# Kernel optimization log

Measured on AMD Instinct MI355X. Metric: run time of the kernel, lower is better.

## Reference

```python
import jax, jax.numpy as jnp
import numpy as np

D_MODEL = 2048
N_HEADS = 16
HEAD_DIM = D_MODEL // N_HEADS
ROPE_THETA = 10000.0
B, S = 2, 2048
MAX_POS = 8192


def _rope(x, position_ids):
    # x: [b, h, s, hd]; position_ids: [b, s] int
    half = HEAD_DIM // 2
    inv_freq = 1.0 / (ROPE_THETA ** (jnp.arange(0, HEAD_DIM, 2, dtype=jnp.float32) / HEAD_DIM))  # [half]
    ang = position_ids[..., None].astype(jnp.float32) * inv_freq  # [b, s, half]
    cos = jnp.concatenate([jnp.cos(ang), jnp.cos(ang)], axis=-1)[:, None]  # [b, 1, s, hd]
    sin = jnp.concatenate([jnp.sin(ang), jnp.sin(ang)], axis=-1)[:, None]
    x1, x2 = x[..., :half], x[..., half:]
    rot = jnp.concatenate([-x2, x1], axis=-1)  # rotate_half
    return x * cos + rot * sin


def setup_inputs() -> dict:
    key = jax.random.key(0)
    ks = jax.random.split(key, 6)
    wscale = 1.0 / np.sqrt(D_MODEL)
    x_sparse = jax.random.normal(ks[0], (B, S, D_MODEL), dtype=jnp.float32)
    Wq = jax.random.normal(ks[1], (D_MODEL, D_MODEL), dtype=jnp.float32) * wscale
    Wk = jax.random.normal(ks[2], (D_MODEL, D_MODEL), dtype=jnp.float32) * wscale
    Wv = jax.random.normal(ks[3], (D_MODEL, D_MODEL), dtype=jnp.float32) * wscale
    Wo = jax.random.normal(ks[4], (D_MODEL, D_MODEL), dtype=jnp.float32) * wscale
    position_ids = jnp.sort(jax.random.randint(ks[5], (B, S), 0, MAX_POS), axis=-1).astype(jnp.int64)
    return {"x_sparse": x_sparse, "Wq": Wq, "Wk": Wk, "Wv": Wv, "Wo": Wo, "position_ids": position_ids}


def reference(x_sparse, Wq, Wk, Wv, Wo, position_ids):
    b, s, d = x_sparse.shape

    def heads(W):
        return (x_sparse @ W).reshape(b, s, N_HEADS, HEAD_DIM).transpose(0, 2, 1, 3)  # [b,h,s,hd]

    q = _rope(heads(Wq), position_ids)
    k = _rope(heads(Wk), position_ids)
    v = heads(Wv)

    scores = jnp.einsum('bhqd,bhkd->bhqk', q, k) / np.float32(np.sqrt(HEAD_DIM))
    # dynamic position-based causal mask: pos_i >= pos_j, broadcast over heads
    mask = position_ids[:, None, :, None] >= position_ids[:, None, None, :]  # [b,1,s,s]
    scores = jnp.where(mask, scores, jnp.float32(-1e30))
    attn = jax.nn.softmax(scores, axis=-1)
    out = jnp.einsum('bhqk,bhkd->bhqd', attn, v)  # [b,h,s,hd]
    out = out.transpose(0, 2, 1, 3).reshape(b, s, d)
    return out @ Wo
```

## Files before the change

kernel.cpp:

```cpp
#include <hip/hip_runtime.h>
#include <stdint.h>


typedef unsigned short u16;
typedef unsigned int u32;
typedef __attribute__((ext_vector_type(8))) short bf16x8;
typedef __attribute__((ext_vector_type(4))) float f32x4;

#define SEQ 2048
#define DM 2048
#define NH 16
#define HD 128
#define SM_SCALE 0.08838834764831845f
#define K2LOG 0.12751743f

__device__ __forceinline__ u16 f2bf(float f) {
  union { float f; uint32_t u; } v; v.f = f;
  uint32_t u = v.u + 0x7fffu + ((v.u >> 16) & 1u);
  return (u16)(u >> 16);
}
__device__ __forceinline__ float bf2f(u16 h) {
  union { uint32_t u; float f; } v; v.u = ((uint32_t)h) << 16; return v.f;
}
__device__ __forceinline__ u32 pack2(float a, float b) {
  return (u32)f2bf(a) | ((u32)f2bf(b) << 16);
}
__device__ __forceinline__ u32 pack2_trunc(float a, float b) {
  union { float f; u32 u; } x, y; x.f = a; y.f = b;
  return (x.u >> 16) | (y.u & 0xFFFF0000u);
}

__device__ __forceinline__ void gl2lds16(const void* g, void* l) {
  __builtin_amdgcn_global_load_lds(
      (const __attribute__((address_space(1))) uint32_t*)g,
      (__attribute__((address_space(3))) uint32_t*)l, 16, 0, 0);
}

__global__ __launch_bounds__(256) void cvt_x(const float* __restrict__ x, u16* __restrict__ xb) {
  int i = blockIdx.x * 256 + threadIdx.x;
  float4 v = ((const float4*)x)[i];
  uint2 r;
  r.x = pack2(v.x, v.y);
  r.y = pack2(v.z, v.w);
  ((uint2*)xb)[i] = r;
}

__global__ __launch_bounds__(256) void wtrans(const float* __restrict__ w0, const float* __restrict__ w1,
                                              const float* __restrict__ w2, const float* __restrict__ w3,
                                              u16* __restrict__ dst) {
  const float* W = blockIdx.z == 0 ? w0 : blockIdx.z == 1 ? w1 : blockIdx.z == 2 ? w2 : w3;
  u16* D = dst + (size_t)blockIdx.z * DM * DM;
  int k0 = blockIdx.x * 32, n0 = blockIdx.y * 32;
  __shared__ u16 t[32][33];
  int tx = threadIdx.x, ty = threadIdx.y;
#pragma unroll
  for (int i = 0; i < 32; i += 8)
    t[ty + i][tx] = f2bf(W[(size_t)(k0 + ty + i) * DM + n0 + tx]);
  __syncthreads();
#pragma unroll
  for (int i = 0; i < 32; i += 8)
    D[(size_t)(n0 + ty + i) * DM + k0 + tx] = t[tx][ty + i];
}

__device__ __forceinline__ void gemm_core(const u16* __restrict__ A, const u16* __restrict__ Bt,
                                          int m0, int n0, u16* As, u16* Bs, f32x4 acc[4][4]) {
  int tid = threadIdx.x, lane = tid & 63;
  int l15 = lane & 15, quad = lane >> 4;
  int wave = tid >> 6;
  int wm = (wave >> 1) * 64, wn = (wave & 1) * 64;
  for (int k0 = 0; k0 < DM; k0 += 64) {
#pragma unroll
    for (int i = 0; i < 4; ++i) {
      int s = i * 256 + tid;
      int row = s >> 3, c = (s & 7) ^ (row & 7);
      gl2lds16(&A[(size_t)(m0 + row) * DM + k0 + c * 8], &As[(s & ~63) * 8]);
      gl2lds16(&Bt[(size_t)(n0 + row) * DM + k0 + c * 8], &Bs[(s & ~63) * 8]);
    }
    __syncthreads();
#pragma unroll
    for (int kk = 0; kk < 2; ++kk) {
      bf16x8 af[4], bfr[4];
#pragma unroll
      for (int mt = 0; mt < 4; ++mt) {
        int row = wm + mt * 16 + l15;
        int c = (kk * 4 + quad) ^ (row & 7);
        af[mt] = *(const bf16x8*)&As[row * 64 + c * 8];
      }
#pragma unroll
      for (int nt = 0; nt < 4; ++nt) {
        int row = wn + nt * 16 + l15;
        int c = (kk * 4 + quad) ^ (row & 7);
        bfr[nt] = *(const bf16x8*)&Bs[row * 64 + c * 8];
      }
#pragma unroll
      for (int mt = 0; mt < 4; ++mt)
#pragma unroll
        for (int nt = 0; nt < 4; ++nt)
          acc[mt][nt] = __builtin_amdgcn_mfma_f32_16x16x32_bf16(af[mt], bfr[nt], acc[mt][nt], 0, 0, 0);
    }
    __syncthreads();
  }
}

__global__ __launch_bounds__(256) void qkv_gemm(const u16* __restrict__ X, const u16* __restrict__ Wt,
                                                u16* __restrict__ Qo, u16* __restrict__ Ko,
                                                u16* __restrict__ Vto) {
  __shared__ u16 As[128 * 64];
  __shared__ u16 Bs[128 * 64];
  const u16* Bt = Wt + (size_t)blockIdx.z * DM * DM;
  int n0 = blockIdx.x * 128, m0 = blockIdx.y * 128;
  f32x4 acc[4][4] = {};
  gemm_core(X, Bt, m0, n0, As, Bs, acc);
  int lane = threadIdx.x & 63, wave = threadIdx.x >> 6;
  int l15 = lane & 15, quad = lane >> 4;
  int wm = (wave >> 1) * 64, wn = (wave & 1) * 64;
  if (blockIdx.z == 2) {
    int h = n0 >> 7;
#pragma unroll
    for (int mt = 0; mt < 4; ++mt)
#pragma unroll
      for (int nt = 0; nt < 4; ++nt) {
        int tok = m0 + wm + mt * 16 + quad * 4;
        int d = wn + nt * 16 + l15;
        int b = tok >> 11, sx = tok & (SEQ - 1);
        u16* dp = &Vto[((size_t)(b * NH + h) * HD + d) * SEQ + sx];
        *(u32*)&dp[0] = pack2(acc[mt][nt][0], acc[mt][nt][1]);
        *(u32*)&dp[2] = pack2(acc[mt][nt][2], acc[mt][nt][3]);
      }
  } else {
    u16* C = blockIdx.z == 0 ? Qo : Ko;
#pragma unroll
    for (int mt = 0; mt < 4; ++mt)
#pragma unroll
      for (int nt = 0; nt < 4; ++nt)
#pragma unroll
        for (int r = 0; r < 4; ++r)
          C[(size_t)(m0 + wm + mt * 16 + quad * 4 + r) * DM + n0 + wn + nt * 16 + l15]
              = f2bf(acc[mt][nt][r]);
  }
}

__global__ __launch_bounds__(256) void proj_gemm(const u16* __restrict__ A, const u16* __restrict__ Wt,
                                                 float* __restrict__ C) {
  __shared__ u16 As[128 * 64];
  __shared__ u16 Bs[128 * 64];
  int n0 = blockIdx.x * 128, m0 = blockIdx.y * 128;
  f32x4 acc[4][4] = {};
  gemm_core(A, Wt, m0, n0, As, Bs, acc);
  int lane = threadIdx.x & 63, wave = threadIdx.x >> 6;
  int l15 = lane & 15, quad = lane >> 4;
  int wm = (wave >> 1) * 64, wn = (wave & 1) * 64;
#pragma unroll
  for (int mt = 0; mt < 4; ++mt)
#pragma unroll
    for (int nt = 0; nt < 4; ++nt)
#pragma unroll
      for (int r = 0; r < 4; ++r)
        C[(size_t)(m0 + wm + mt * 16 + quad * 4 + r) * DM + n0 + wn + nt * 16 + l15] = acc[mt][nt][r];
}

__global__ __launch_bounds__(256) void rope_k(u16* __restrict__ Q, u16* __restrict__ K,
                                              const int* __restrict__ pos) {
  uint32_t idx = blockIdx.x * 256 + threadIdx.x;
  int i = idx & 63;
  int h = (idx >> 6) & 15;
  int s = (idx >> 10) & 2047;
  int b = idx >> 21;
  u16* P = (blockIdx.y == 0) ? Q : K;
  int p = pos[b * SEQ + s];
  float inv_rev = exp2f(fmaf((float)i, -0.20762051f, -2.6514961f));
  float pf = (float)p;
  float hi = pf * inv_rev;
  float err = fmaf(pf, inv_rev, -hi);
  float r = (hi - truncf(hi)) + err;
  float ang = r * 6.2831853f;
  float sn = __sinf(ang), cs = __cosf(ang);
  size_t base = ((size_t)(b * SEQ + s)) * DM + h * HD;
  float x1 = bf2f(P[base + i]), x2 = bf2f(P[base + 64 + i]);
  P[base + i] = f2bf(x1 * cs - x2 * sn);
  P[base + 64 + i] = f2bf(x2 * cs + x1 * sn);
}

__global__ __launch_bounds__(256, 2) void attn_k(const u16* __restrict__ Q, const u16* __restrict__ K,
                                                 const u16* __restrict__ Vt, const int* __restrict__ pos,
                                                 u16* __restrict__ AO) {
  int tid = threadIdx.x, lane = tid & 63, wave = tid >> 6;
  int x = blockIdx.x & 7;
  int g = blockIdx.x >> 3;
  int bh = x + 8 * wave;
  int stripe = (g < 32) ? (2 * g) : (127 - 2 * g);
  int b = bh >> 4, h = bh & 15;
  int l15 = lane & 15, quad = lane >> 4;
  const int* posb = pos + b * SEQ;
  int qbase = stripe * 32;
  const u16* Kbase = &K[(size_t)(b * SEQ) * DM + h * HD];
  const u16* Vbase = &Vt[(size_t)(b * NH + h) * HD * SEQ];

  bf16x8 qf[2][4];
#pragma unroll
  for (int qi = 0; qi < 2; ++qi)
#pragma unroll
    for (int kk = 0; kk < 4; ++kk)
      qf[qi][kk] = *(const bf16x8*)&Q[(size_t)(b * SEQ + qbase + qi * 16 + l15) * DM
                                      + h * HD + kk * 32 + quad * 8];

  auto ub = [&](int v) {
    int c = 0;
#pragma unroll
    for (int st = 1024; st; st >>= 1)
      if (posb[c + st - 1] <= v) c += st;
    if (c == 2047 && posb[2047] <= v) c = 2048;
    return c;
  };
  int cnt[2];
  cnt[0] = ub(posb[qbase + l15]);
  cnt[1] = ub(posb[qbase + 16 + l15]);
  int cnt_min = ub(posb[qbase]);
  int cnt_max = ub(posb[qbase + 31]);
  int ntile = (cnt_max + 63) >> 6;

  float m_i[2] = {-1.0e30f, -1.0e30f}, l_i[2] = {0.0f, 0.0f};
  f32x4 oacc[2][8] = {};

  int base0 = l15 + ((quad & 1) << 5);
  bool hi_sel = (quad >> 1) != 0;

  for (int j = 0; j < ntile; ++j) {
    int j0 = j * 64;
    bf16x8 kf[4][4];
#pragma unroll
    for (int kk = 0; kk < 4; ++kk)
#pragma unroll
      for (int kt = 0; kt < 4; ++kt)
        kf[kk][kt] = *(const bf16x8*)&Kbase[(size_t)(j0 + kt * 16 + l15) * DM + kk * 32 + quad * 8];

    f32x4 sacc[2][4] = {};
#pragma unroll
    for (int kk = 0; kk < 4; ++kk)
#pragma unroll
      for (int qi = 0; qi < 2; ++qi)
#pragma unroll
        for (int kt = 0; kt < 4; ++kt)
          sacc[qi][kt] = __builtin_amdgcn_mfma_f32_16x16x32_bf16(kf[kk][kt], qf[qi][kk], sacc[qi][kt], 0, 0, 0);

    bf16x8 vf[2][8];
#pragma unroll
    for (int kk2 = 0; kk2 < 2; ++kk2)
#pragma unroll
      for (int dt = 0; dt < 8; ++dt)
        vf[kk2][dt] = *(const bf16x8*)&Vbase[(size_t)(dt * 16 + l15) * SEQ + j0 + kk2 * 32 + quad * 8];

    bool need_mask = (j0 + 64 > cnt_min);
    u32 pb[2][4][2];
#pragma unroll
    for (int qi = 0; qi < 2; ++qi) {
      if (need_mask) {
        int rel = cnt[qi] - j0;
#pragma unroll
        for (int kt = 0; kt < 4; ++kt)
#pragma unroll
          for (int r = 0; r < 4; ++r)
            if (kt * 16 + quad * 4 + r >= rel) sacc[qi][kt][r] = -1.0e30f;
      }
      float mx = fmaxf(fmaxf(sacc[qi][0][0], sacc[qi][0][1]), fmaxf(sacc[qi][0][2], sacc[qi][0][3]));
#pragma unroll
      for (int kt = 1; kt < 4; ++kt)
        mx = fmaxf(mx, fmaxf(fmaxf(sacc[qi][kt][0], sacc[qi][kt][1]),
                             fmaxf(sacc[qi][kt][2], sacc[qi][kt][3])));
      mx = fmaxf(mx, __shfl_xor(mx, 16));
      mx = fmaxf(mx, __shfl_xor(mx, 32));
      float mold = m_i[qi];
      float mn = fmaxf(mold, mx);
      if (__any(mn > mold)) {
        float al = exp2f((mold - mn) * K2LOG);
        l_i[qi] *= al;
#pragma unroll
        for (int dt = 0; dt < 8; ++dt) oacc[qi][dt] *= al;
        m_i[qi] = mn;
      }
      float nc = -m_i[qi] * K2LOG;
      float rs = 0.0f;
#pragma unroll
      for (int kt = 0; kt < 4; ++kt) {
        float p0 = exp2f(fmaf(sacc[qi][kt][0], K2LOG, nc));
        float p1 = exp2f(fmaf(sacc[qi][kt][1], K2LOG, nc));
        float p2 = exp2f(fmaf(sacc[qi][kt][2], K2LOG, nc));
        float p3 = exp2f(fmaf(sacc[qi][kt][3], K2LOG, nc));
        rs += (p0 + p1) + (p2 + p3);
        pb[qi][kt][0] = pack2_trunc(p0, p1);
        pb[qi][kt][1] = pack2_trunc(p2, p3);
      }
      rs += __shfl_xor(rs, 16);
      rs += __shfl_xor(rs, 32);
      l_i[qi] += rs;
    }

#pragma unroll
    for (int kk2 = 0; kk2 < 2; ++kk2) {
#pragma unroll
      for (int qi = 0; qi < 2; ++qi) {
        u32 w[4];
#pragma unroll
        for (int wd = 0; wd < 4; ++wd) {
          int src = base0 + ((wd >> 1) << 4);
          u32 va = __shfl(pb[qi][kk2 * 2 + 0][wd & 1], src);
          u32 vb = __shfl(pb[qi][kk2 * 2 + 1][wd & 1], src);
          w[wd] = hi_sel ? vb : va;
        }
        union { bf16x8 v; u32 u[4]; } pt;
        pt.u[0] = w[0]; pt.u[1] = w[1]; pt.u[2] = w[2]; pt.u[3] = w[3];
#pragma unroll
        for (int dt = 0; dt < 8; ++dt)
          oacc[qi][dt] = __builtin_amdgcn_mfma_f32_16x16x32_bf16(vf[kk2][dt], pt.v, oacc[qi][dt], 0, 0, 0);
      }
    }
  }

#pragma unroll
  for (int qi = 0; qi < 2; ++qi) {
    float inv = 1.0f / l_i[qi];
    u16* aop = &AO[(size_t)(b * SEQ + qbase + qi * 16 + l15) * DM + h * HD];
#pragma unroll
    for (int dt = 0; dt < 8; ++dt) {
      int col = dt * 16 + quad * 4;
      *(u32*)&aop[col]     = pack2(oacc[qi][dt][0] * inv, oacc[qi][dt][1] * inv);
      *(u32*)&aop[col + 2] = pack2(oacc[qi][dt][2] * inv, oacc[qi][dt][3] * inv);
    }
  }
}

extern "C" void kernel_launch(void* const* d_in, const int* in_sizes, int n_in,
                              void* d_out, int out_size, void* d_ws, size_t ws_size,
                              hipStream_t stream) {
  const float* x  = (const float*)d_in[0];
  const float* Wq = (const float*)d_in[1];
  const float* Wk = (const float*)d_in[2];
  const float* Wv = (const float*)d_in[3];
  const float* Wo = (const float*)d_in[4];
  const int*  pos = (const int*)d_in[5];
  float* out = (float*)d_out;

  u16* ws  = (u16*)d_ws;
  u16* xb  = ws;
  u16* wt  = xb  + (size_t)4096 * 2048;
  u16* qb  = wt  + (size_t)4 * 2048 * 2048;
  u16* kb  = qb  + (size_t)4096 * 2048;
  u16* vtb = kb  + (size_t)4096 * 2048;
  u16* aob = vtb + (size_t)4096 * 2048;

  cvt_x<<<8192, 256, 0, stream>>>(x, xb);
  wtrans<<<dim3(64, 64, 4), dim3(32, 8), 0, stream>>>(Wq, Wk, Wv, Wo, wt);
  qkv_gemm<<<dim3(16, 32, 3), 256, 0, stream>>>(xb, wt, qb, kb, vtb);
  rope_k<<<dim3(16384, 2), 256, 0, stream>>>(qb, kb, pos);
  attn_k<<<dim3(512), 256, 0, stream>>>(qb, kb, vtb, pos, aob);
  proj_gemm<<<dim3(16, 32), 256, 0, stream>>>(aob, wt + (size_t)3 * 2048 * 2048, out);
}
```

Measured before the change: 461.9 us.

## Split attention KV range across wave pairs and merge partial softmax in LDS

The attention kernel now gives each block two query stripes, one early and one late, with two waves per stripe. Each wave of a pair processes half of the KV tiles, and the partial max, sum and output accumulators are merged through shared memory before the write. This doubles the number of blocks, raises the occupancy target in launch bounds and evens out the causal work, at the cost of an LDS reduction, extra syncs and possible register pressure or spills. The QKV GEMM grid is also flattened from a 3D to a 2D grid that indexes the stacked transposed weights directly.

```diff
diff --git a/kernel.cpp b/kernel.cpp
--- a/kernel.cpp
+++ b/kernel.cpp
@@ -107,15 +107,15 @@
                                                 u16* __restrict__ Vto) {
   __shared__ u16 As[128 * 64];
   __shared__ u16 Bs[128 * 64];
-  const u16* Bt = Wt + (size_t)blockIdx.z * DM * DM;
   int n0 = blockIdx.x * 128, m0 = blockIdx.y * 128;
   f32x4 acc[4][4] = {};
-  gemm_core(X, Bt, m0, n0, As, Bs, acc);
+  gemm_core(X, Wt, m0, n0, As, Bs, acc);
   int lane = threadIdx.x & 63, wave = threadIdx.x >> 6;
   int l15 = lane & 15, quad = lane >> 4;
   int wm = (wave >> 1) * 64, wn = (wave & 1) * 64;
-  if (blockIdx.z == 2) {
-    int h = n0 >> 7;
+  int z = n0 >> 11;
+  if (z == 2) {
+    int h = (n0 >> 7) & 15;
 #pragma unroll
     for (int mt = 0; mt < 4; ++mt)
 #pragma unroll
@@ -128,14 +128,15 @@
         *(u32*)&dp[2] = pack2(acc[mt][nt][2], acc[mt][nt][3]);
       }
   } else {
-    u16* C = blockIdx.z == 0 ? Qo : Ko;
+    u16* C = z == 0 ? Qo : Ko;
+    int nl = n0 & (DM - 1);
 #pragma unroll
     for (int mt = 0; mt < 4; ++mt)
 #pragma unroll
       for (int nt = 0; nt < 4; ++nt)
 #pragma unroll
         for (int r = 0; r < 4; ++r)
-          C[(size_t)(m0 + wm + mt * 16 + quad * 4 + r) * DM + n0 + wn + nt * 16 + l15]
+          C[(size_t)(m0 + wm + mt * 16 + quad * 4 + r) * DM + nl + wn + nt * 16 + l15]
               = f2bf(acc[mt][nt][r]);
   }
 }
@@ -181,14 +182,17 @@
   P[base + 64 + i] = f2bf(x2 * cs + x1 * sn);
 }
 
-__global__ __launch_bounds__(256, 2) void attn_k(const u16* __restrict__ Q, const u16* __restrict__ K,
+__global__ __launch_bounds__(256, 4) void attn_k(const u16* __restrict__ Q, const u16* __restrict__ K,
                                                  const u16* __restrict__ Vt, const int* __restrict__ pos,
                                                  u16* __restrict__ AO) {
+  __shared__ f32x4 Ol[2][2][8][64];
+  __shared__ float Ml[2][2][64], Ll[2][2][64];
   int tid = threadIdx.x, lane = tid & 63, wave = tid >> 6;
-  int x = blockIdx.x & 7;
-  int g = blockIdx.x >> 3;
-  int bh = x + 8 * wave;
-  int stripe = (g < 32) ? (2 * g) : (127 - 2 * g);
+  int beta = blockIdx.x;
+  int bh = beta & 31;
+  int gamma = beta >> 5;
+  int stripe = (wave < 2) ? gamma : (63 - gamma);
+  int half = wave & 1, pair = wave >> 1;
   int b = bh >> 4, h = bh & 15;
   int l15 = lane & 15, quad = lane >> 4;
   const int* posb = pos + b * SEQ;
@@ -218,6 +222,9 @@
   int cnt_min = ub(posb[qbase]);
   int cnt_max = ub(posb[qbase + 31]);
   int ntile = (cnt_max + 63) >> 6;
+  int mid = (ntile + 1) >> 1;
+  int jbeg = half ? mid : 0;
+  int jend = half ? ntile : mid;
 
   float m_i[2] = {-1.0e30f, -1.0e30f}, l_i[2] = {0.0f, 0.0f};
   f32x4 oacc[2][8] = {};
@@ -225,7 +232,7 @@
   int base0 = l15 + ((quad & 1) << 5);
   bool hi_sel = (quad >> 1) != 0;
 
-  for (int j = 0; j < ntile; ++j) {
+  for (int j = jbeg; j < jend; ++j) {
     int j0 = j * 64;
     bf16x8 kf[4][4];
 #pragma unroll
@@ -316,15 +323,36 @@
     }
   }
 
-#pragma unroll
-  for (int qi = 0; qi < 2; ++qi) {
-    float inv = 1.0f / l_i[qi];
-    u16* aop = &AO[(size_t)(b * SEQ + qbase + qi * 16 + l15) * DM + h * HD];
-#pragma unroll
-    for (int dt = 0; dt < 8; ++dt) {
-      int col = dt * 16 + quad * 4;
-      *(u32*)&aop[col]     = pack2(oacc[qi][dt][0] * inv, oacc[qi][dt][1] * inv);
-      *(u32*)&aop[col + 2] = pack2(oacc[qi][dt][2] * inv, oacc[qi][dt][3] * inv);
+  __syncthreads();
+  if (half) {
+#pragma unroll
+    for (int qi = 0; qi < 2; ++qi) {
+      Ml[pair][qi][lane] = m_i[qi];
+      Ll[pair][qi][lane] = l_i[qi];
+#pragma unroll
+      for (int dt = 0; dt < 8; ++dt) Ol[pair][qi][dt][lane] = oacc[qi][dt];
+    }
+  }
+  __syncthreads();
+  if (!half) {
+#pragma unroll
+    for (int qi = 0; qi < 2; ++qi) {
+      float m2 = Ml[pair][qi][lane];
+      float l2 = Ll[pair][qi][lane];
+      float mm = fmaxf(m_i[qi], m2);
+      float a1 = exp2f((m_i[qi] - mm) * K2LOG);
+      float a2 = exp2f((m2 - mm) * K2LOG);
+      float inv = 1.0f / (l_i[qi] * a1 + l2 * a2);
+      float s1 = a1 * inv, s2 = a2 * inv;
+      u16* aop = &AO[(size_t)(b * SEQ + qbase + qi * 16 + l15) * DM + h * HD];
+#pragma unroll
+      for (int dt = 0; dt < 8; ++dt) {
+        f32x4 o2 = Ol[pair][qi][dt][lane];
+        f32x4 om = oacc[qi][dt] * s1 + o2 * s2;
+        int col = dt * 16 + quad * 4;
+        *(u32*)&aop[col]     = pack2(om[0], om[1]);
+        *(u32*)&aop[col + 2] = pack2(om[2], om[3]);
+      }
     }
   }
 }
@@ -350,8 +378,8 @@
 
   cvt_x<<<8192, 256, 0, stream>>>(x, xb);
   wtrans<<<dim3(64, 64, 4), dim3(32, 8), 0, stream>>>(Wq, Wk, Wv, Wo, wt);
-  qkv_gemm<<<dim3(16, 32, 3), 256, 0, stream>>>(xb, wt, qb, kb, vtb);
+  qkv_gemm<<<dim3(48, 32), 256, 0, stream>>>(xb, wt, qb, kb, vtb);
   rope_k<<<dim3(16384, 2), 256, 0, stream>>>(qb, kb, pos);
-  attn_k<<<dim3(512), 256, 0, stream>>>(qb, kb, vtb, pos, aob);
+  attn_k<<<dim3(1024), 256, 0, stream>>>(qb, kb, vtb, pos, aob);
   proj_gemm<<<dim3(16, 32), 256, 0, stream>>>(aob, wt + (size_t)3 * 2048 * 2048, out);
 }
```

Result: slower. 785.8 us (+70.1%).
